# Kernel tuning notes

Measured on AMD Instinct MI355X. Metric: run time of the kernel, lower is better.

Reference implementation:

```python
import jax, jax.numpy as jnp
import numpy as np

N = 100000
E = 1600000
D_IN = 128
D_HID = 128
D_HID2 = D_HID // 2  # 64
D_OUT = 1


def _glorot(key, shape):
    fan_in, fan_out = shape[1], shape[0]
    lim = float(np.sqrt(6.0 / (fan_in + fan_out)))
    return jax.random.uniform(key, shape, jnp.float32, -lim, lim)


def setup_inputs() -> dict:
    key = jax.random.key(0)
    ks = jax.random.split(key, 10)
    x = jax.random.normal(ks[0], (N, D_IN), jnp.float32)
    edge_index = jax.random.randint(ks[1], (2, E), 0, N, jnp.int64)
    return {
        "x": x,
        "edge_index": edge_index,
        # SAGEConv1: lin_l acts on mean-aggregated neighbors, lin_r on root
        "W1_l": _glorot(ks[2], (D_HID, D_IN)),
        "W1_r": _glorot(ks[3], (D_HID, D_IN)),
        "b1": jnp.zeros((D_HID,), jnp.float32),
        # SAGEConv2
        "W2_l": _glorot(ks[4], (D_HID2, D_HID)),
        "W2_r": _glorot(ks[5], (D_HID2, D_HID)),
        "b2": jnp.zeros((D_HID2,), jnp.float32),
        # classifier Linear
        "Wc": _glorot(ks[6], (D_OUT, D_HID2)),
        "bc": jnp.zeros((D_OUT,), jnp.float32),
    }


def _sage_conv(x, src, dst, Wl, Wr, b):
    # mean aggregation of source features onto destination nodes
    msg = x[src]  # [E, d] gather
    agg = jax.ops.segment_sum(msg, dst, num_segments=x.shape[0])  # [N, d]
    deg = jax.ops.segment_sum(jnp.ones((src.shape[0],), x.dtype), dst,
                              num_segments=x.shape[0])  # [N]
    agg = agg / jnp.maximum(deg, 1.0)[:, None]
    # out = lin_l(mean_aggr) + lin_r(x) + bias  (PyG SAGEConv default)
    return agg @ Wl.T + x @ Wr.T + b


def reference(x, edge_index, W1_l, W1_r, b1, W2_l, W2_r, b2, Wc, bc):
    src, dst = edge_index[0], edge_index[1]
    h = jax.nn.relu(_sage_conv(x, src, dst, W1_l, W1_r, b1))
    # dropout(p=0.3) is identity in eval mode
    h = jax.nn.relu(_sage_conv(h, src, dst, W2_l, W2_r, b2))
    logits = h @ Wc.T + bc  # [N, 1]
    return logits
```

## Files before the change

kernel.cpp:

```cpp
#include <hip/hip_runtime.h>


static constexpr int TPB = 256;
static constexpr int NWG = 512;
static constexpr int ECMAX = 3200;
static constexpr int NBMAX = 1024;
static constexpr int BCAP = 2560;

typedef __attribute__((ext_vector_type(8))) short bf16x8;
typedef __attribute__((ext_vector_type(4))) float f32x4;
typedef __attribute__((ext_vector_type(2))) float f32x2;

#if __has_builtin(__builtin_amdgcn_cvt_pk_f32_fp8) && __has_builtin(__builtin_amdgcn_cvt_pk_fp8_f32)
#define FP8_HW 1
#endif

__device__ __forceinline__ unsigned short f2bf(float f) {
  union { float f; unsigned u; } v; v.f = f;
  unsigned r = v.u + 0x7FFFu + ((v.u >> 16) & 1u);
  return (unsigned short)(r >> 16);
}
__device__ __forceinline__ float bf2f(unsigned short h) {
  union { unsigned u; float f; } v; v.u = ((unsigned)h) << 16;
  return v.f;
}

__device__ __forceinline__ float fp82f_sw(unsigned u) {
  unsigned e = (u >> 3) & 15u, m = u & 7u;
  float f;
  if (e == 0) f = (float)m * 0.001953125f;
  else {
    union { unsigned u; float f; } v;
    v.u = ((e + 120u) << 23) | (m << 20);
    f = v.f;
  }
  return (u & 0x80u) ? -f : f;
}

__device__ __forceinline__ unsigned char f2fp8(float f) {
#ifdef FP8_HW
  return (unsigned char)(__builtin_amdgcn_cvt_pk_fp8_f32(f, f, 0, false) & 0xFF);
#else
  union { float f; unsigned u; } v; v.f = f;
  unsigned s = (v.u >> 24) & 0x80u;
  unsigned a = v.u & 0x7FFFFFFFu;
  if (a >= 0x43E00000u) return (unsigned char)(s | 0x7Eu);
  int e32 = (int)(a >> 23);
  if (e32 < 121) {
    float sc = __builtin_fabsf(f) * 512.0f;
    int m = (int)(sc + 0.5f);
    if (m >= 8) return (unsigned char)(s | 0x08u);
    return (unsigned char)(s | (unsigned)m);
  }
  unsigned m = a & 0x7FFFFFu;
  unsigned lsb = (m >> 20) & 1u;
  m += 0x7FFFFu + lsb;
  unsigned e8 = (unsigned)(e32 - 120);
  if (m >= 0x800000u) { m -= 0x800000u; e8 += 1; }
  if (e8 >= 16) return (unsigned char)(s | 0x7Eu);
  return (unsigned char)(s | (e8 << 3) | (m >> 20));
#endif
}

__device__ __forceinline__ void fp8x8_acc(uint2 v, float* acc) {
#ifdef FP8_HW
  f32x2 a0 = __builtin_amdgcn_cvt_pk_f32_fp8(v.x, false);
  f32x2 a1 = __builtin_amdgcn_cvt_pk_f32_fp8(v.x, true);
  f32x2 a2 = __builtin_amdgcn_cvt_pk_f32_fp8(v.y, false);
  f32x2 a3 = __builtin_amdgcn_cvt_pk_f32_fp8(v.y, true);
  acc[0] += a0[0]; acc[1] += a0[1]; acc[2] += a1[0]; acc[3] += a1[1];
  acc[4] += a2[0]; acc[5] += a2[1]; acc[6] += a3[0]; acc[7] += a3[1];
#else
  acc[0] += fp82f_sw(v.x & 255); acc[1] += fp82f_sw((v.x >> 8) & 255);
  acc[2] += fp82f_sw((v.x >> 16) & 255); acc[3] += fp82f_sw(v.x >> 24);
  acc[4] += fp82f_sw(v.y & 255); acc[5] += fp82f_sw((v.y >> 8) & 255);
  acc[6] += fp82f_sw((v.y >> 16) & 255); acc[7] += fp82f_sw(v.y >> 24);
#endif
}

__global__ void k_wprep(const float* __restrict__ W1l, const float* __restrict__ W1r,
                        const float* __restrict__ W2l, const float* __restrict__ W2r,
                        unsigned short* __restrict__ wb1l,
                        unsigned short* __restrict__ wb1r,
                        unsigned short* __restrict__ wb2,
                        int* __restrict__ bcur, int NB) {
  int i = blockIdx.x * blockDim.x + threadIdx.x;
  if (i < NB) bcur[i] = 0;
  if (i < 16384) wb1l[i] = f2bf(W1l[i]);
  else if (i < 32768) wb1r[i - 16384] = f2bf(W1r[i - 16384]);
  else if (i < 40960) wb2[i - 32768] = f2bf(W2l[i - 32768]);
  else if (i < 49152) wb2[8192 + i - 40960] = f2bf(W2r[i - 40960]);
}

__global__ __launch_bounds__(TPB) void k_bscatter(
    const int* __restrict__ src, const int* __restrict__ dst,
    int* __restrict__ bcur, int* __restrict__ ebuf, int E, int NB, int EC) {
  __shared__ int pv[ECMAX];
  __shared__ unsigned short kb[ECMAX];
  __shared__ int lhist[NBMAX];
  __shared__ int lcur[NBMAX];
  int t = threadIdx.x;
  for (int b = t; b < NB; b += TPB) lhist[b] = 0;
  int base = blockIdx.x * EC;
  int cnt = min(EC, E - base);
  __syncthreads();
  for (int i = t; i < cnt; i += TPB) {
    int sv = src[base + i], dv = dst[base + i];
    int b = dv >> 7;
    kb[i] = (unsigned short)b;
    pv[i] = ((dv & 127) << 17) | sv;
    atomicAdd(&lhist[b], 1);
  }
  __syncthreads();
  for (int b = t; b < NB; b += TPB) {
    int c = lhist[b];
    lcur[b] = c ? (b * BCAP + atomicAdd(&bcur[b], c)) : 0;
  }
  __syncthreads();
  for (int i = t; i < cnt; i += TPB) {
    int b = kb[i];
    int pos = atomicAdd(&lcur[b], 1);
    if (pos < (b + 1) * BCAP) ebuf[pos] = pv[i];
  }
}

__global__ __launch_bounds__(TPB) void k_bcsr(
    const int* __restrict__ ebuf, const int* __restrict__ bcur,
    int* __restrict__ rowptr, int* __restrict__ col, int N, int NB) {
  __shared__ int deg[128], sscan[128], lcur[128], red[TPB];
  int b = blockIdx.x, t = threadIdx.x;
  int part = 0;
  for (int i = t; i < b; i += TPB) part += min(bcur[i], BCAP);
  red[t] = part; __syncthreads();
  for (int off = TPB / 2; off > 0; off >>= 1) {
    if (t < off) red[t] += red[t + off];
    __syncthreads();
  }
  int e0 = red[0];
  int mycnt = min(bcur[b], BCAP);
  int e1 = e0 + mycnt;
  int ebase = b * BCAP;
  if (t < 128) deg[t] = 0;
  __syncthreads();
  for (int i = t; i < mycnt; i += TPB)
    atomicAdd(&deg[ebuf[ebase + i] >> 17], 1);
  __syncthreads();
  if (t < 128) sscan[t] = deg[t];
  __syncthreads();
  for (int off = 1; off < 128; off <<= 1) {
    int x = 0;
    if (t < 128 && t >= off) x = sscan[t - off];
    __syncthreads();
    if (t < 128) sscan[t] += x;
    __syncthreads();
  }
  if (t < 128) {
    int excl = sscan[t] - deg[t];
    int node0 = (b << 7) + t;
    if (node0 < N) rowptr[node0] = e0 + excl;
    lcur[t] = e0 + excl;
  }
  if (b == NB - 1 && t == 0) rowptr[N] = e1;
  __syncthreads();
  for (int i = t; i < mycnt; i += TPB) {
    int pvv = ebuf[ebase + i];
    int pos = atomicAdd(&lcur[pvv >> 17], 1);
    col[pos] = pvv & 0x1FFFF;
  }
}

static constexpr int LD = 136;

__global__ __launch_bounds__(TPB, 4) void k_lin1(
    const float* __restrict__ X, const unsigned short* __restrict__ wl,
    const unsigned short* __restrict__ wr, unsigned char* __restrict__ t1,
    unsigned short* __restrict__ r1, int N) {
  __shared__ unsigned short As[64 * LD];
  int t = threadIdx.x;
  int row0 = blockIdx.x * 64;
  for (int i = t; i < 64 * 32; i += TPB) {
    int r = i >> 5, k4 = i & 31;
    int gr = row0 + r;
    float4 v;
    if (gr < N) v = *(const float4*)&X[(size_t)gr * 128 + k4 * 4];
    else { v.x = v.y = v.z = v.w = 0.f; }
    ushort4 o; o.x = f2bf(v.x); o.y = f2bf(v.y); o.z = f2bf(v.z); o.w = f2bf(v.w);
    *(ushort4*)&As[r * LD + k4 * 4] = o;
  }
  __syncthreads();
  int w = t >> 6, l = t & 63;
  int lr = l & 15, lk = l >> 4;
  f32x4 at[4][2], ar[4][2];
#pragma unroll
  for (int mb = 0; mb < 4; ++mb)
#pragma unroll
    for (int nb = 0; nb < 2; ++nb)
#pragma unroll
      for (int q = 0; q < 4; ++q) { at[mb][nb][q] = 0.f; ar[mb][nb][q] = 0.f; }
#pragma unroll
  for (int ks = 0; ks < 4; ++ks) {
    int koff = ks * 32 + lk * 8;
    bf16x8 a[4], bl[2], br[2];
#pragma unroll
    for (int mb = 0; mb < 4; ++mb)
      a[mb] = *(const bf16x8*)&As[(mb * 16 + lr) * LD + koff];
#pragma unroll
    for (int nb = 0; nb < 2; ++nb) {
      int c = w * 32 + nb * 16 + lr;
      bl[nb] = *(const bf16x8*)&wl[c * 128 + koff];
      br[nb] = *(const bf16x8*)&wr[c * 128 + koff];
    }
#pragma unroll
    for (int mb = 0; mb < 4; ++mb)
#pragma unroll
      for (int nb = 0; nb < 2; ++nb) {
        at[mb][nb] = __builtin_amdgcn_mfma_f32_16x16x32_bf16(a[mb], bl[nb], at[mb][nb], 0, 0, 0);
        ar[mb][nb] = __builtin_amdgcn_mfma_f32_16x16x32_bf16(a[mb], br[nb], ar[mb][nb], 0, 0, 0);
      }
  }
#pragma unroll
  for (int mb = 0; mb < 4; ++mb) {
    int r = row0 + mb * 16 + lk * 4;
#pragma unroll
    for (int nb = 0; nb < 2; ++nb) {
      int c = w * 32 + nb * 16 + lr;
#pragma unroll
      for (int j = 0; j < 4; ++j) {
        if (r + j < N) {
          t1[(size_t)(r + j) * 128 + c] = f2fp8(at[mb][nb][j]);
          r1[(size_t)(r + j) * 128 + c] = f2bf(ar[mb][nb][j]);
        }
      }
    }
  }
}

__global__ __launch_bounds__(TPB, 4) void k_lin2(
    const unsigned short* __restrict__ h1, const unsigned short* __restrict__ w2,
    unsigned char* __restrict__ y2, unsigned short* __restrict__ r2, int N) {
  __shared__ unsigned short As[64 * LD];
  int t = threadIdx.x;
  int row0 = blockIdx.x * 64;
  for (int i = t * 8; i < 64 * 128; i += TPB * 8) {
    int r = i >> 7, k8 = i & 127;
    int gr = row0 + r;
    bf16x8 v;
    if (gr < N) v = *(const bf16x8*)&h1[(size_t)gr * 128 + k8];
    else { for (int q = 0; q < 8; ++q) v[q] = 0; }
    *(bf16x8*)&As[r * LD + k8] = v;
  }
  __syncthreads();
  int w = t >> 6, l = t & 63;
  int lr = l & 15, lk = l >> 4;
  f32x4 acc[4][2];
#pragma unroll
  for (int mb = 0; mb < 4; ++mb)
#pragma unroll
    for (int nb = 0; nb < 2; ++nb)
#pragma unroll
      for (int q = 0; q < 4; ++q) acc[mb][nb][q] = 0.f;
#pragma unroll
  for (int ks = 0; ks < 4; ++ks) {
    int koff = ks * 32 + lk * 8;
    bf16x8 a[4], bfr[2];
#pragma unroll
    for (int mb = 0; mb < 4; ++mb)
      a[mb] = *(const bf16x8*)&As[(mb * 16 + lr) * LD + koff];
#pragma unroll
    for (int nb = 0; nb < 2; ++nb) {
      int c = w * 32 + nb * 16 + lr;
      bfr[nb] = *(const bf16x8*)&w2[c * 128 + koff];
    }
#pragma unroll
    for (int mb = 0; mb < 4; ++mb)
#pragma unroll
      for (int nb = 0; nb < 2; ++nb)
        acc[mb][nb] = __builtin_amdgcn_mfma_f32_16x16x32_bf16(a[mb], bfr[nb], acc[mb][nb], 0, 0, 0);
  }
#pragma unroll
  for (int mb = 0; mb < 4; ++mb) {
    int r = row0 + mb * 16 + lk * 4;
#pragma unroll
    for (int nb = 0; nb < 2; ++nb) {
      int c = w * 32 + nb * 16 + lr;
#pragma unroll
      for (int j = 0; j < 4; ++j) {
        if (r + j < N) {
          if (c < 64) y2[(size_t)(r + j) * 64 + c] = f2fp8(acc[mb][nb][j]);
          else        r2[(size_t)(r + j) * 64 + (c - 64)] = f2bf(acc[mb][nb][j]);
        }
      }
    }
  }
}

__global__ void k_aggh1(const unsigned char* __restrict__ t1,
                        const unsigned short* __restrict__ r1,
                        const int* __restrict__ rowptr, const int* __restrict__ col,
                        const float* __restrict__ b1,
                        unsigned short* __restrict__ h1, int n) {
  int wid = (int)(((size_t)blockIdx.x * blockDim.x + threadIdx.x) >> 6);
  int l = threadIdx.x & 63;
  if (wid >= n) return;
  int rp0 = rowptr[wid], rp1 = rowptr[wid + 1];
  int g = l >> 4, s = l & 15;
  float acc[8];
#pragma unroll
  for (int q = 0; q < 8; ++q) acc[q] = 0.f;
  int j = rp0 + g;
  for (; j + 12 < rp1; j += 16) {
    int c0 = col[j], c1 = col[j + 4], c2 = col[j + 8], c3 = col[j + 12];
    uint2 v0 = *(const uint2*)&t1[(size_t)c0 * 128 + s * 8];
    uint2 v1 = *(const uint2*)&t1[(size_t)c1 * 128 + s * 8];
    uint2 v2 = *(const uint2*)&t1[(size_t)c2 * 128 + s * 8];
    uint2 v3 = *(const uint2*)&t1[(size_t)c3 * 128 + s * 8];
    fp8x8_acc(v0, acc); fp8x8_acc(v1, acc);
    fp8x8_acc(v2, acc); fp8x8_acc(v3, acc);
  }
  for (; j + 4 < rp1; j += 8) {
    int c0 = col[j], c1 = col[j + 4];
    uint2 v0 = *(const uint2*)&t1[(size_t)c0 * 128 + s * 8];
    uint2 v1 = *(const uint2*)&t1[(size_t)c1 * 128 + s * 8];
    fp8x8_acc(v0, acc); fp8x8_acc(v1, acc);
  }
  if (j < rp1) {
    uint2 v0 = *(const uint2*)&t1[(size_t)col[j] * 128 + s * 8];
    fp8x8_acc(v0, acc);
  }
#pragma unroll
  for (int q = 0; q < 8; ++q) {
    acc[q] += __shfl_xor(acc[q], 16, 64);
    acc[q] += __shfl_xor(acc[q], 32, 64);
  }
  if (g == 0) {
    int d = rp1 - rp0;
    float inv = 1.f / (float)(d > 1 ? d : 1);
    bf16x8 rr = *(const bf16x8*)&r1[(size_t)wid * 128 + s * 8];
    float4 bb0 = *(const float4*)&b1[s * 8];
    float4 bb1 = *(const float4*)&b1[s * 8 + 4];
    float bbv[8] = {bb0.x, bb0.y, bb0.z, bb0.w, bb1.x, bb1.y, bb1.z, bb1.w};
    bf16x8 o;
#pragma unroll
    for (int q = 0; q < 8; ++q) {
      float h = acc[q] * inv + bf2f((unsigned short)rr[q]) + bbv[q];
      h = h > 0.f ? h : 0.f;
      o[q] = (short)f2bf(h);
    }
    *(bf16x8*)&h1[(size_t)wid * 128 + s * 8] = o;
  }
}

__global__ void k_agghead(const unsigned char* __restrict__ y2,
                          const unsigned short* __restrict__ r2,
                          const int* __restrict__ rowptr, const int* __restrict__ col,
                          const float* __restrict__ b2, const float* __restrict__ Wc,
                          const float* __restrict__ bc, float* __restrict__ out, int n) {
  int wid = (int)(((size_t)blockIdx.x * blockDim.x + threadIdx.x) >> 6);
  int l = threadIdx.x & 63;
  if (wid >= n) return;
  int rp0 = rowptr[wid], rp1 = rowptr[wid + 1];
  int g = l >> 3, s = l & 7;
  float acc[8];
#pragma unroll
  for (int q = 0; q < 8; ++q) acc[q] = 0.f;
  int j = rp0 + g;
  for (; j + 8 < rp1; j += 16) {
    int c0 = col[j], c1 = col[j + 8];
    uint2 v0 = *(const uint2*)&y2[(size_t)c0 * 64 + s * 8];
    uint2 v1 = *(const uint2*)&y2[(size_t)c1 * 64 + s * 8];
    fp8x8_acc(v0, acc); fp8x8_acc(v1, acc);
  }
  if (j < rp1) {
    uint2 v0 = *(const uint2*)&y2[(size_t)col[j] * 64 + s * 8];
    fp8x8_acc(v0, acc);
  }
#pragma unroll
  for (int q = 0; q < 8; ++q) {
    acc[q] += __shfl_xor(acc[q], 8, 64);
    acc[q] += __shfl_xor(acc[q], 16, 64);
    acc[q] += __shfl_xor(acc[q], 32, 64);
  }
  if (g == 0) {
    int d = rp1 - rp0;
    float inv = 1.f / (float)(d > 1 ? d : 1);
    bf16x8 rr = *(const bf16x8*)&r2[(size_t)wid * 64 + s * 8];
    float4 bb0 = *(const float4*)&b2[s * 8];
    float4 bb1 = *(const float4*)&b2[s * 8 + 4];
    float bbv[8] = {bb0.x, bb0.y, bb0.z, bb0.w, bb1.x, bb1.y, bb1.z, bb1.w};
    float4 wc0 = *(const float4*)&Wc[s * 8];
    float4 wc1 = *(const float4*)&Wc[s * 8 + 4];
    float wcv[8] = {wc0.x, wc0.y, wc0.z, wc0.w, wc1.x, wc1.y, wc1.z, wc1.w};
    float p = 0.f;
#pragma unroll
    for (int q = 0; q < 8; ++q) {
      float h = acc[q] * inv + bf2f((unsigned short)rr[q]) + bbv[q];
      h = h > 0.f ? h : 0.f;
      p += h * wcv[q];
    }
    p += __shfl_xor(p, 1, 64);
    p += __shfl_xor(p, 2, 64);
    p += __shfl_xor(p, 4, 64);
    if (s == 0) out[wid] = p + bc[0];
  }
}

extern "C" void kernel_launch(void* const* d_in, const int* in_sizes, int n_in,
                              void* d_out, int out_size, void* d_ws, size_t ws_size,
                              hipStream_t stream) {
  const float* x   = (const float*)d_in[0];
  const int*   ei  = (const int*)d_in[1];
  const float* W1l = (const float*)d_in[2];
  const float* W1r = (const float*)d_in[3];
  const float* b1  = (const float*)d_in[4];
  const float* W2l = (const float*)d_in[5];
  const float* W2r = (const float*)d_in[6];
  const float* b2  = (const float*)d_in[7];
  const float* Wc  = (const float*)d_in[8];
  const float* bc  = (const float*)d_in[9];
  float* logits = (float*)d_out;

  const int N = in_sizes[0] / 128;
  const int E = in_sizes[1] / 2;
  const int NB = (N + 127) >> 7;
  const int EC = (E + NWG - 1) / NWG;

  char* ws = (char*)d_ws;
  size_t o = 0;
  auto alloc = [&](size_t bytes) { size_t r = o; o += (bytes + 511) & ~511ULL; return r; };
  size_t o_rp    = alloc((size_t)(N + 1) * 4);
  size_t o_bcur  = alloc((size_t)NB * 4);
  size_t o_col   = alloc((size_t)E * 4);
  size_t o_ebuf  = alloc((size_t)NB * BCAP * 4);
  size_t o_wb    = alloc((size_t)(3 * 128 * 128) * 2);
  size_t o_t1    = alloc((size_t)N * 128);
  size_t o_r1    = alloc((size_t)N * 128 * 2);
  size_t o_h1    = alloc((size_t)N * 128 * 2);
  size_t o_y2    = alloc((size_t)N * 64);
  size_t o_r2    = alloc((size_t)N * 64 * 2);
  if (o > ws_size) return;

  int* rp    = (int*)(ws + o_rp);
  int* bcur  = (int*)(ws + o_bcur);
  int* col   = (int*)(ws + o_col);
  int* ebuf  = (int*)(ws + o_ebuf);
  unsigned short* wb1l = (unsigned short*)(ws + o_wb);
  unsigned short* wb1r = wb1l + 128 * 128;
  unsigned short* wb2  = wb1r + 128 * 128;
  unsigned char*  t1 = (unsigned char*)(ws + o_t1);
  unsigned short* r1 = (unsigned short*)(ws + o_r1);
  unsigned short* h1 = (unsigned short*)(ws + o_h1);
  unsigned char*  y2 = (unsigned char*)(ws + o_y2);
  unsigned short* r2 = (unsigned short*)(ws + o_r2);

  const int* esrc = ei;
  const int* edst = ei + E;

  int gtiles = (N + 63) / 64;
  int nodeblocks = (int)(((size_t)N * 64 + TPB - 1) / TPB);

  k_wprep<<<192, TPB, 0, stream>>>(W1l, W1r, W2l, W2r, wb1l, wb1r, wb2, bcur, NB);
  k_lin1<<<gtiles, TPB, 0, stream>>>(x, wb1l, wb1r, t1, r1, N);
  k_bscatter<<<NWG, TPB, 0, stream>>>(esrc, edst, bcur, ebuf, E, NB, EC);
  k_bcsr<<<NB, TPB, 0, stream>>>(ebuf, bcur, rp, col, N, NB);
  k_aggh1<<<nodeblocks, TPB, 0, stream>>>(t1, r1, rp, col, b1, h1, N);
  k_lin2<<<gtiles, TPB, 0, stream>>>(h1, wb2, y2, r2, N);
  k_agghead<<<nodeblocks, TPB, 0, stream>>>(y2, r2, rp, col, b2, Wc, bc, logits, N);
}
```

Baseline: 188.2 us.

## Merge lin1 GEMM and edge bucket scatter into one launch; pack fp8 accumulators

```diff
diff --git a/kernel.cpp b/kernel.cpp
--- a/kernel.cpp
+++ b/kernel.cpp
@@ -62,19 +62,17 @@
 #endif
 }
 
-__device__ __forceinline__ void fp8x8_acc(uint2 v, float* acc) {
+__device__ __forceinline__ void fp8x8_acc2(uint2 v, f32x2* a) {
 #ifdef FP8_HW
-  f32x2 a0 = __builtin_amdgcn_cvt_pk_f32_fp8(v.x, false);
-  f32x2 a1 = __builtin_amdgcn_cvt_pk_f32_fp8(v.x, true);
-  f32x2 a2 = __builtin_amdgcn_cvt_pk_f32_fp8(v.y, false);
-  f32x2 a3 = __builtin_amdgcn_cvt_pk_f32_fp8(v.y, true);
-  acc[0] += a0[0]; acc[1] += a0[1]; acc[2] += a1[0]; acc[3] += a1[1];
-  acc[4] += a2[0]; acc[5] += a2[1]; acc[6] += a3[0]; acc[7] += a3[1];
+  a[0] += __builtin_amdgcn_cvt_pk_f32_fp8(v.x, false);
+  a[1] += __builtin_amdgcn_cvt_pk_f32_fp8(v.x, true);
+  a[2] += __builtin_amdgcn_cvt_pk_f32_fp8(v.y, false);
+  a[3] += __builtin_amdgcn_cvt_pk_f32_fp8(v.y, true);
 #else
-  acc[0] += fp82f_sw(v.x & 255); acc[1] += fp82f_sw((v.x >> 8) & 255);
-  acc[2] += fp82f_sw((v.x >> 16) & 255); acc[3] += fp82f_sw(v.x >> 24);
-  acc[4] += fp82f_sw(v.y & 255); acc[5] += fp82f_sw((v.y >> 8) & 255);
-  acc[6] += fp82f_sw((v.y >> 16) & 255); acc[7] += fp82f_sw(v.y >> 24);
+  a[0][0] += fp82f_sw(v.x & 255); a[0][1] += fp82f_sw((v.x >> 8) & 255);
+  a[1][0] += fp82f_sw((v.x >> 16) & 255); a[1][1] += fp82f_sw(v.x >> 24);
+  a[2][0] += fp82f_sw(v.y & 255); a[2][1] += fp82f_sw((v.y >> 8) & 255);
+  a[3][0] += fp82f_sw((v.y >> 16) & 255); a[3][1] += fp82f_sw(v.y >> 24);
 #endif
 }
 
@@ -92,35 +90,103 @@
   else if (i < 49152) wb2[8192 + i - 40960] = f2bf(W2r[i - 40960]);
 }
 
-__global__ __launch_bounds__(TPB) void k_bscatter(
+static constexpr int LD = 136;
+static constexpr int SMEM_INTS = 6848;
+
+__global__ __launch_bounds__(TPB, 4) void k_lin1_bsc(
+    const float* __restrict__ X, const unsigned short* __restrict__ wl,
+    const unsigned short* __restrict__ wr, unsigned char* __restrict__ t1,
+    unsigned short* __restrict__ r1, int N,
     const int* __restrict__ src, const int* __restrict__ dst,
     int* __restrict__ bcur, int* __restrict__ ebuf, int E, int NB, int EC) {
-  __shared__ int pv[ECMAX];
-  __shared__ unsigned short kb[ECMAX];
-  __shared__ int lhist[NBMAX];
-  __shared__ int lcur[NBMAX];
+  __shared__ int smem[SMEM_INTS];
+  int bid = blockIdx.x;
   int t = threadIdx.x;
-  for (int b = t; b < NB; b += TPB) lhist[b] = 0;
-  int base = blockIdx.x * EC;
-  int cnt = min(EC, E - base);
-  __syncthreads();
-  for (int i = t; i < cnt; i += TPB) {
-    int sv = src[base + i], dv = dst[base + i];
-    int b = dv >> 7;
-    kb[i] = (unsigned short)b;
-    pv[i] = ((dv & 127) << 17) | sv;
-    atomicAdd(&lhist[b], 1);
-  }
-  __syncthreads();
-  for (int b = t; b < NB; b += TPB) {
-    int c = lhist[b];
-    lcur[b] = c ? (b * BCAP + atomicAdd(&bcur[b], c)) : 0;
-  }
-  __syncthreads();
-  for (int i = t; i < cnt; i += TPB) {
-    int b = kb[i];
-    int pos = atomicAdd(&lcur[b], 1);
-    if (pos < (b + 1) * BCAP) ebuf[pos] = pv[i];
+  if (bid < NWG) {
+    int* pv = smem;
+    unsigned short* kb = (unsigned short*)(smem + ECMAX);
+    int* lhist = smem + ECMAX + ((ECMAX + 1) >> 1);
+    int* lcur  = lhist + NBMAX;
+    for (int b = t; b < NB; b += TPB) lhist[b] = 0;
+    int base = bid * EC;
+    int cnt = min(EC, E - base);
+    __syncthreads();
+    for (int i = t; i < cnt; i += TPB) {
+      int sv = src[base + i], dv = dst[base + i];
+      int b = dv >> 7;
+      kb[i] = (unsigned short)b;
+      pv[i] = ((dv & 127) << 17) | sv;
+      atomicAdd(&lhist[b], 1);
+    }
+    __syncthreads();
+    for (int b = t; b < NB; b += TPB) {
+      int c = lhist[b];
+      lcur[b] = c ? (b * BCAP + atomicAdd(&bcur[b], c)) : 0;
+    }
+    __syncthreads();
+    for (int i = t; i < cnt; i += TPB) {
+      int b = kb[i];
+      int pos = atomicAdd(&lcur[b], 1);
+      if (pos < (b + 1) * BCAP) ebuf[pos] = pv[i];
+    }
+    return;
+  }
+  unsigned short* As = (unsigned short*)smem;
+  int row0 = (bid - NWG) * 64;
+  for (int i = t; i < 64 * 32; i += TPB) {
+    int r = i >> 5, k4 = i & 31;
+    int gr = row0 + r;
+    float4 v;
+    if (gr < N) v = *(const float4*)&X[(size_t)gr * 128 + k4 * 4];
+    else { v.x = v.y = v.z = v.w = 0.f; }
+    ushort4 o; o.x = f2bf(v.x); o.y = f2bf(v.y); o.z = f2bf(v.z); o.w = f2bf(v.w);
+    *(ushort4*)&As[r * LD + k4 * 4] = o;
+  }
+  __syncthreads();
+  int w = t >> 6, l = t & 63;
+  int lr = l & 15, lk = l >> 4;
+  f32x4 at[4][2], ar[4][2];
+#pragma unroll
+  for (int mb = 0; mb < 4; ++mb)
+#pragma unroll
+    for (int nb = 0; nb < 2; ++nb)
+#pragma unroll
+      for (int q = 0; q < 4; ++q) { at[mb][nb][q] = 0.f; ar[mb][nb][q] = 0.f; }
+#pragma unroll
+  for (int ks = 0; ks < 4; ++ks) {
+    int koff = ks * 32 + lk * 8;
+    bf16x8 a[4], bl[2], br[2];
+#pragma unroll
+    for (int mb = 0; mb < 4; ++mb)
+      a[mb] = *(const bf16x8*)&As[(mb * 16 + lr) * LD + koff];
+#pragma unroll
+    for (int nb = 0; nb < 2; ++nb) {
+      int c = w * 32 + nb * 16 + lr;
+      bl[nb] = *(const bf16x8*)&wl[c * 128 + koff];
+      br[nb] = *(const bf16x8*)&wr[c * 128 + koff];
+    }
+#pragma unroll
+    for (int mb = 0; mb < 4; ++mb)
+#pragma unroll
+      for (int nb = 0; nb < 2; ++nb) {
+        at[mb][nb] = __builtin_amdgcn_mfma_f32_16x16x32_bf16(a[mb], bl[nb], at[mb][nb], 0, 0, 0);
+        ar[mb][nb] = __builtin_amdgcn_mfma_f32_16x16x32_bf16(a[mb], br[nb], ar[mb][nb], 0, 0, 0);
+      }
+  }
+#pragma unroll
+  for (int mb = 0; mb < 4; ++mb) {
+    int r = row0 + mb * 16 + lk * 4;
+#pragma unroll
+    for (int nb = 0; nb < 2; ++nb) {
+      int c = w * 32 + nb * 16 + lr;
+#pragma unroll
+      for (int j = 0; j < 4; ++j) {
+        if (r + j < N) {
+          t1[(size_t)(r + j) * 128 + c] = f2fp8(at[mb][nb][j]);
+          r1[(size_t)(r + j) * 128 + c] = f2bf(ar[mb][nb][j]);
+        }
+      }
+    }
   }
 }
 
@@ -169,69 +235,61 @@
   }
 }
 
-static constexpr int LD = 136;
-
-__global__ __launch_bounds__(TPB, 4) void k_lin1(
-    const float* __restrict__ X, const unsigned short* __restrict__ wl,
-    const unsigned short* __restrict__ wr, unsigned char* __restrict__ t1,
-    unsigned short* __restrict__ r1, int N) {
-  __shared__ unsigned short As[64 * LD];
-  int t = threadIdx.x;
-  int row0 = blockIdx.x * 64;
-  for (int i = t; i < 64 * 32; i += TPB) {
-    int r = i >> 5, k4 = i & 31;
-    int gr = row0 + r;
-    float4 v;
-    if (gr < N) v = *(const float4*)&X[(size_t)gr * 128 + k4 * 4];
-    else { v.x = v.y = v.z = v.w = 0.f; }
-    ushort4 o; o.x = f2bf(v.x); o.y = f2bf(v.y); o.z = f2bf(v.z); o.w = f2bf(v.w);
-    *(ushort4*)&As[r * LD + k4 * 4] = o;
-  }
-  __syncthreads();
-  int w = t >> 6, l = t & 63;
-  int lr = l & 15, lk = l >> 4;
-  f32x4 at[4][2], ar[4][2];
-#pragma unroll
-  for (int mb = 0; mb < 4; ++mb)
-#pragma unroll
-    for (int nb = 0; nb < 2; ++nb)
-#pragma unroll
-      for (int q = 0; q < 4; ++q) { at[mb][nb][q] = 0.f; ar[mb][nb][q] = 0.f; }
-#pragma unroll
-  for (int ks = 0; ks < 4; ++ks) {
-    int koff = ks * 32 + lk * 8;
-    bf16x8 a[4], bl[2], br[2];
-#pragma unroll
-    for (int mb = 0; mb < 4; ++mb)
-      a[mb] = *(const bf16x8*)&As[(mb * 16 + lr) * LD + koff];
-#pragma unroll
-    for (int nb = 0; nb < 2; ++nb) {
-      int c = w * 32 + nb * 16 + lr;
-      bl[nb] = *(const bf16x8*)&wl[c * 128 + koff];
-      br[nb] = *(const bf16x8*)&wr[c * 128 + koff];
-    }
-#pragma unroll
-    for (int mb = 0; mb < 4; ++mb)
-#pragma unroll
-      for (int nb = 0; nb < 2; ++nb) {
-        at[mb][nb] = __builtin_amdgcn_mfma_f32_16x16x32_bf16(a[mb], bl[nb], at[mb][nb], 0, 0, 0);
-        ar[mb][nb] = __builtin_amdgcn_mfma_f32_16x16x32_bf16(a[mb], br[nb], ar[mb][nb], 0, 0, 0);
-      }
-  }
-#pragma unroll
-  for (int mb = 0; mb < 4; ++mb) {
-    int r = row0 + mb * 16 + lk * 4;
-#pragma unroll
-    for (int nb = 0; nb < 2; ++nb) {
-      int c = w * 32 + nb * 16 + lr;
-#pragma unroll
-      for (int j = 0; j < 4; ++j) {
-        if (r + j < N) {
-          t1[(size_t)(r + j) * 128 + c] = f2fp8(at[mb][nb][j]);
-          r1[(size_t)(r + j) * 128 + c] = f2bf(ar[mb][nb][j]);
-        }
-      }
-    }
+__global__ void k_aggh1(const unsigned char* __restrict__ t1,
+                        const unsigned short* __restrict__ r1,
+                        const int* __restrict__ rowptr, const int* __restrict__ col,
+                        const float* __restrict__ b1,
+                        unsigned short* __restrict__ h1, int n) {
+  int wid = (int)(((size_t)blockIdx.x * blockDim.x + threadIdx.x) >> 6);
+  int l = threadIdx.x & 63;
+  if (wid >= n) return;
+  int rp0 = rowptr[wid], rp1 = rowptr[wid + 1];
+  int g = l >> 4, s = l & 15;
+  f32x2 acc2[4];
+#pragma unroll
+  for (int q = 0; q < 4; ++q) { acc2[q][0] = 0.f; acc2[q][1] = 0.f; }
+  int j = rp0 + g;
+  for (; j + 12 < rp1; j += 16) {
+    int c0 = col[j], c1 = col[j + 4], c2 = col[j + 8], c3 = col[j + 12];
+    uint2 v0 = *(const uint2*)&t1[(size_t)c0 * 128 + s * 8];
+    uint2 v1 = *(const uint2*)&t1[(size_t)c1 * 128 + s * 8];
+    uint2 v2 = *(const uint2*)&t1[(size_t)c2 * 128 + s * 8];
+    uint2 v3 = *(const uint2*)&t1[(size_t)c3 * 128 + s * 8];
+    fp8x8_acc2(v0, acc2); fp8x8_acc2(v1, acc2);
+    fp8x8_acc2(v2, acc2); fp8x8_acc2(v3, acc2);
+  }
+  for (; j + 4 < rp1; j += 8) {
+    int c0 = col[j], c1 = col[j + 4];
+    uint2 v0 = *(const uint2*)&t1[(size_t)c0 * 128 + s * 8];
+    uint2 v1 = *(const uint2*)&t1[(size_t)c1 * 128 + s * 8];
+    fp8x8_acc2(v0, acc2); fp8x8_acc2(v1, acc2);
+  }
+  if (j < rp1) {
+    uint2 v0 = *(const uint2*)&t1[(size_t)col[j] * 128 + s * 8];
+    fp8x8_acc2(v0, acc2);
+  }
+#pragma unroll
+  for (int q = 0; q < 4; ++q)
+#pragma unroll
+    for (int k = 0; k < 2; ++k) {
+      acc2[q][k] += __shfl_xor(acc2[q][k], 16, 64);
+      acc2[q][k] += __shfl_xor(acc2[q][k], 32, 64);
+    }
+  if (g == 0) {
+    int d = rp1 - rp0;
+    float inv = 1.f / (float)(d > 1 ? d : 1);
+    bf16x8 rr = *(const bf16x8*)&r1[(size_t)wid * 128 + s * 8];
+    float4 bb0 = *(const float4*)&b1[s * 8];
+    float4 bb1 = *(const float4*)&b1[s * 8 + 4];
+    float bbv[8] = {bb0.x, bb0.y, bb0.z, bb0.w, bb1.x, bb1.y, bb1.z, bb1.w};
+    bf16x8 o;
+#pragma unroll
+    for (int q = 0; q < 8; ++q) {
+      float h = acc2[q >> 1][q & 1] * inv + bf2f((unsigned short)rr[q]) + bbv[q];
+      h = h > 0.f ? h : 0.f;
+      o[q] = (short)f2bf(h);
+    }
+    *(bf16x8*)&h1[(size_t)wid * 128 + s * 8] = o;
   }
 }
 
@@ -294,62 +352,6 @@
   }
 }
 
-__global__ void k_aggh1(const unsigned char* __restrict__ t1,
-                        const unsigned short* __restrict__ r1,
-                        const int* __restrict__ rowptr, const int* __restrict__ col,
-                        const float* __restrict__ b1,
-                        unsigned short* __restrict__ h1, int n) {
-  int wid = (int)(((size_t)blockIdx.x * blockDim.x + threadIdx.x) >> 6);
-  int l = threadIdx.x & 63;
-  if (wid >= n) return;
-  int rp0 = rowptr[wid], rp1 = rowptr[wid + 1];
-  int g = l >> 4, s = l & 15;
-  float acc[8];
-#pragma unroll
-  for (int q = 0; q < 8; ++q) acc[q] = 0.f;
-  int j = rp0 + g;
-  for (; j + 12 < rp1; j += 16) {
-    int c0 = col[j], c1 = col[j + 4], c2 = col[j + 8], c3 = col[j + 12];
-    uint2 v0 = *(const uint2*)&t1[(size_t)c0 * 128 + s * 8];
-    uint2 v1 = *(const uint2*)&t1[(size_t)c1 * 128 + s * 8];
-    uint2 v2 = *(const uint2*)&t1[(size_t)c2 * 128 + s * 8];
-    uint2 v3 = *(const uint2*)&t1[(size_t)c3 * 128 + s * 8];
-    fp8x8_acc(v0, acc); fp8x8_acc(v1, acc);
-    fp8x8_acc(v2, acc); fp8x8_acc(v3, acc);
-  }
-  for (; j + 4 < rp1; j += 8) {
-    int c0 = col[j], c1 = col[j + 4];
-    uint2 v0 = *(const uint2*)&t1[(size_t)c0 * 128 + s * 8];
-    uint2 v1 = *(const uint2*)&t1[(size_t)c1 * 128 + s * 8];
-    fp8x8_acc(v0, acc); fp8x8_acc(v1, acc);
-  }
-  if (j < rp1) {
-    uint2 v0 = *(const uint2*)&t1[(size_t)col[j] * 128 + s * 8];
-    fp8x8_acc(v0, acc);
-  }
-#pragma unroll
-  for (int q = 0; q < 8; ++q) {
-    acc[q] += __shfl_xor(acc[q], 16, 64);
-    acc[q] += __shfl_xor(acc[q], 32, 64);
-  }
-  if (g == 0) {
-    int d = rp1 - rp0;
-    float inv = 1.f / (float)(d > 1 ? d : 1);
-    bf16x8 rr = *(const bf16x8*)&r1[(size_t)wid * 128 + s * 8];
-    float4 bb0 = *(const float4*)&b1[s * 8];
-    float4 bb1 = *(const float4*)&b1[s * 8 + 4];
-    float bbv[8] = {bb0.x, bb0.y, bb0.z, bb0.w, bb1.x, bb1.y, bb1.z, bb1.w};
-    bf16x8 o;
-#pragma unroll
-    for (int q = 0; q < 8; ++q) {
-      float h = acc[q] * inv + bf2f((unsigned short)rr[q]) + bbv[q];
-      h = h > 0.f ? h : 0.f;
-      o[q] = (short)f2bf(h);
-    }
-    *(bf16x8*)&h1[(size_t)wid * 128 + s * 8] = o;
-  }
-}
-
 __global__ void k_agghead(const unsigned char* __restrict__ y2,
                           const unsigned short* __restrict__ r2,
                           const int* __restrict__ rowptr, const int* __restrict__ col,
@@ -360,26 +362,28 @@
   if (wid >= n) return;
   int rp0 = rowptr[wid], rp1 = rowptr[wid + 1];
   int g = l >> 3, s = l & 7;
-  float acc[8];
-#pragma unroll
-  for (int q = 0; q < 8; ++q) acc[q] = 0.f;
+  f32x2 acc2[4];
+#pragma unroll
+  for (int q = 0; q < 4; ++q) { acc2[q][0] = 0.f; acc2[q][1] = 0.f; }
   int j = rp0 + g;
   for (; j + 8 < rp1; j += 16) {
     int c0 = col[j], c1 = col[j + 8];
     uint2 v0 = *(const uint2*)&y2[(size_t)c0 * 64 + s * 8];
     uint2 v1 = *(const uint2*)&y2[(size_t)c1 * 64 + s * 8];
-    fp8x8_acc(v0, acc); fp8x8_acc(v1, acc);
+    fp8x8_acc2(v0, acc2); fp8x8_acc2(v1, acc2);
   }
   if (j < rp1) {
     uint2 v0 = *(const uint2*)&y2[(size_t)col[j] * 64 + s * 8];
-    fp8x8_acc(v0, acc);
-  }
-#pragma unroll
-  for (int q = 0; q < 8; ++q) {
-    acc[q] += __shfl_xor(acc[q], 8, 64);
-    acc[q] += __shfl_xor(acc[q], 16, 64);
-    acc[q] += __shfl_xor(acc[q], 32, 64);
-  }
+    fp8x8_acc2(v0, acc2);
+  }
+#pragma unroll
+  for (int q = 0; q < 4; ++q)
+#pragma unroll
+    for (int k = 0; k < 2; ++k) {
+      acc2[q][k] += __shfl_xor(acc2[q][k], 8, 64);
+      acc2[q][k] += __shfl_xor(acc2[q][k], 16, 64);
+      acc2[q][k] += __shfl_xor(acc2[q][k], 32, 64);
+    }
   if (g == 0) {
     int d = rp1 - rp0;
     float inv = 1.f / (float)(d > 1 ? d : 1);
@@ -393,7 +397,7 @@
     float p = 0.f;
 #pragma unroll
     for (int q = 0; q < 8; ++q) {
-      float h = acc[q] * inv + bf2f((unsigned short)rr[q]) + bbv[q];
+      float h = acc2[q >> 1][q & 1] * inv + bf2f((unsigned short)rr[q]) + bbv[q];
       h = h > 0.f ? h : 0.f;
       p += h * wcv[q];
     }
@@ -459,8 +463,8 @@
   int nodeblocks = (int)(((size_t)N * 64 + TPB - 1) / TPB);
 
   k_wprep<<<192, TPB, 0, stream>>>(W1l, W1r, W2l, W2r, wb1l, wb1r, wb2, bcur, NB);
-  k_lin1<<<gtiles, TPB, 0, stream>>>(x, wb1l, wb1r, t1, r1, N);
-  k_bscatter<<<NWG, TPB, 0, stream>>>(esrc, edst, bcur, ebuf, E, NB, EC);
+  k_lin1_bsc<<<NWG + gtiles, TPB, 0, stream>>>(
+      x, wb1l, wb1r, t1, r1, N, esrc, edst, bcur, ebuf, E, NB, EC);
   k_bcsr<<<NB, TPB, 0, stream>>>(ebuf, bcur, rp, col, N, NB);
   k_aggh1<<<nodeblocks, TPB, 0, stream>>>(t1, r1, rp, col, b1, h1, N);
   k_lin2<<<gtiles, TPB, 0, stream>>>(h1, wb2, y2, r2, N);
```

Result: no change. 185.0 us (-1.7%).
